# Optimization experiments

Measured on AMD Instinct MI355X. Metric: run time of the kernel, lower is better.

Reference implementation:

```python
import jax, jax.numpy as jnp
import numpy as np

E4M3_MAX = 448.0  # fp8_max_fwd for Format.HYBRID fprop tensors
MARGIN = 0        # DelayedScaling default


def _quantize_e4m3(t, s):
    # cast_to_fp8: scale, saturate-cast to E4M3; amax of the unscaled tensor
    q = (t * s).astype(jnp.float8_e4m3fn)
    amax = jnp.max(jnp.abs(t))
    return q, amax


def _sf_compute(amax, scale, fp8_max, margin):
    # faithful port of _default_sf_compute (including its tf.where ordering)
    exp = jnp.floor(jnp.log2(fp8_max / amax)) - margin
    sf = jnp.round(jnp.exp2(jnp.abs(exp)))
    sf = jnp.where(amax > 0.0, sf, scale)
    sf = jnp.where(jnp.isinf(amax), sf, scale)
    sf = jnp.where(exp < 0, 1.0 / sf, sf)
    return sf


def setup_inputs() -> dict:
    key = jax.random.key(0)
    k1, k2 = jax.random.split(key)
    M, K, N = 16384, 2048, 2048
    x = jax.random.normal(k1, (M, K), dtype=jnp.float32)
    kernel = jax.random.normal(k2, (K, N), dtype=jnp.float32) * 0.02
    scale = jnp.ones((2,), dtype=jnp.float32)
    scale_inv = jnp.ones((2,), dtype=jnp.float32)
    amax_history = jnp.zeros((1, 2), dtype=jnp.float32)
    return {"x": x, "kernel": kernel, "scale": scale,
            "scale_inv": scale_inv, "amax_history": amax_history}


def reference(x, kernel, scale, scale_inv, amax_history):
    # --- cast_to_fp8 for activation (index 0) and weight (index 1) ---
    x_q, amax_x = _quantize_e4m3(x, scale[0])          # [M, K] fp8
    w_q, amax_w = _quantize_e4m3(kernel.T, scale[1])   # [N, K] fp8 (B in row-major, gemm does B^T)
    new_scale_inv = jnp.stack([1.0 / scale[0], 1.0 / scale[1]])
    # record amaxes into most-recent slot of the history
    amax_history = amax_history.at[0, 0].set(amax_x).at[0, 1].set(amax_w)

    # --- fp8_matmul: D = (A * A_scale_inv) @ (B * B_scale_inv)^T ---
    out = jnp.matmul(x_q.astype(jnp.float32), w_q.astype(jnp.float32).T)
    out = out * (new_scale_inv[0] * new_scale_inv[1])  # [M, N]

    # --- fused_amax_and_scale_update (amax_compute_algo='most_recent') ---
    amax = amax_history[0]
    rolled = jnp.roll(amax_history, -1, axis=0).at[0].set(0.0)
    new_scale = _sf_compute(amax, scale, E4M3_MAX, MARGIN)
    return out, new_scale, rolled
```

## Files before the change

kernel.cpp:

```cpp
#include <hip/hip_runtime.h>
#include <cstdint>

#define M_DIM 16384
#define K_DIM 2048
#define N_DIM 2048

typedef float f32x4 __attribute__((ext_vector_type(4)));
typedef int   i32x8 __attribute__((ext_vector_type(8)));

__global__ __launch_bounds__(256) void quant_x_kernel(
    const float4* __restrict__ x, uint4* __restrict__ xq,
    const float* __restrict__ scale, unsigned int* __restrict__ amax)
{
    const int gid = blockIdx.x * 256 + threadIdx.x;
    const float s = scale[0];
    float m = 0.0f;
#pragma unroll
    for (int j = 0; j < 8; ++j) {
        float4 v = x[gid + j * 1048576];
        m = fmaxf(m, fmaxf(fmaxf(fabsf(v.x), fabsf(v.y)),
                           fmaxf(fabsf(v.z), fabsf(v.w))));
        unsigned int p0 = __builtin_amdgcn_cvt_pk_fp8_f32(v.x * s, v.y * s, 0, false);
        unsigned int p  = __builtin_amdgcn_cvt_pk_fp8_f32(v.z * s, v.w * s, p0, true);
        ((unsigned int*)xq)[gid + j * 1048576] = p;
    }

#pragma unroll
    for (int off = 32; off > 0; off >>= 1)
        m = fmaxf(m, __shfl_down(m, off, 64));
    __shared__ float red[4];
    if ((threadIdx.x & 63) == 0) red[threadIdx.x >> 6] = m;
    __syncthreads();
    if (threadIdx.x == 0) {
        m = fmaxf(fmaxf(red[0], red[1]), fmaxf(red[2], red[3]));
        atomicMax(amax, __float_as_uint(m));
    }
}

__global__ __launch_bounds__(256) void quant_w_kernel(
    const float* __restrict__ w, uint8_t* __restrict__ wq,
    const float* __restrict__ scale, unsigned int* __restrict__ amax)
{
    __shared__ float tile[64][68];
    const int t = threadIdx.x;
    const int nb = blockIdx.x * 64;
    const int kb = blockIdx.y * 64;
    const float s = scale[1];
    float m = 0.0f;
#pragma unroll
    for (int j = 0; j < 4; ++j) {
        int f = j * 256 + t;
        int row = f >> 4;
        int c4 = f & 15;
        float4 v = *(const float4*)(w + (size_t)(kb + row) * N_DIM + nb + c4 * 4);
        m = fmaxf(m, fmaxf(fmaxf(fabsf(v.x), fabsf(v.y)),
                           fmaxf(fabsf(v.z), fabsf(v.w))));
        *(float4*)(&tile[row][c4 * 4]) = v;
    }
    __syncthreads();
    const int n = t >> 2, c = t & 3;
    unsigned int pk[4];
#pragma unroll
    for (int jj = 0; jj < 4; ++jj) {
        float f0 = tile[c * 16 + jj * 4 + 0][n] * s;
        float f1 = tile[c * 16 + jj * 4 + 1][n] * s;
        float f2 = tile[c * 16 + jj * 4 + 2][n] * s;
        float f3 = tile[c * 16 + jj * 4 + 3][n] * s;
        unsigned int p = __builtin_amdgcn_cvt_pk_fp8_f32(f0, f1, 0, false);
        pk[jj] = __builtin_amdgcn_cvt_pk_fp8_f32(f2, f3, p, true);
    }
    *(uint4*)(wq + (size_t)(nb + n) * K_DIM + kb + c * 16) = make_uint4(pk[0], pk[1], pk[2], pk[3]);

#pragma unroll
    for (int off = 32; off > 0; off >>= 1)
        m = fmaxf(m, __shfl_down(m, off, 64));
    __shared__ float red[4];
    if ((t & 63) == 0) red[t >> 6] = m;
    __syncthreads();
    if (t == 0) {
        m = fmaxf(fmaxf(red[0], red[1]), fmaxf(red[2], red[3]));
        atomicMax(amax, __float_as_uint(m));
    }
}

__global__ __launch_bounds__(256) void gemm_fp8_kernel(
    const uint8_t* __restrict__ Aq, const uint8_t* __restrict__ Bq,
    const float* __restrict__ scale, float* __restrict__ C)
{
    __shared__ uint8_t lA[16384];
    __shared__ uint8_t lB[16384];
    const int tid  = threadIdx.x;
    const int wave = tid >> 6;
    const int lane = tid & 63;
    const int wm = wave >> 1, wn = wave & 1;
    const int q = lane >> 4, r = lane & 15;

    const int bn = blockIdx.x;
    const int bm = blockIdx.y;
    const size_t a_base = (size_t)bm * 128 * K_DIM;
    const size_t b_base = (size_t)bn * 128 * K_DIM;

    int srow[4], skoff[4], sdst[4];
#pragma unroll
    for (int j = 0; j < 4; ++j) {
        const int s  = j * 4 + wave;
        const int g  = s >> 1, hh = s & 1;
        const int fl = hh * 32 + (lane >> 1);
        srow[j]  = g * 16 + (fl & 15);
        skoff[j] = (fl >> 4) * 32 + (lane & 1) * 16;
        sdst[j]  = s * 1024 + lane * 16;
    }

    f32x4 acc[4][4];
#pragma unroll
    for (int i = 0; i < 4; ++i)
#pragma unroll
        for (int j = 0; j < 4; ++j) acc[i][j] = (f32x4){0.f, 0.f, 0.f, 0.f};

    const int SONE = 0x7F7F7F7F;

    for (int kt = 0; kt < K_DIM / 128; ++kt) {
        __syncthreads();
        const size_t kg = (size_t)kt * 128;
#pragma unroll
        for (int j = 0; j < 4; ++j) {
            const uint8_t* ga = Aq + a_base + (size_t)srow[j] * K_DIM + kg + skoff[j];
            const uint8_t* gb = Bq + b_base + (size_t)srow[j] * K_DIM + kg + skoff[j];
            __builtin_amdgcn_global_load_lds(
                (const __attribute__((address_space(1))) uint32_t*)ga,
                (__attribute__((address_space(3))) uint32_t*)(lA + sdst[j]), 16, 0, 0);
            __builtin_amdgcn_global_load_lds(
                (const __attribute__((address_space(1))) uint32_t*)gb,
                (__attribute__((address_space(3))) uint32_t*)(lB + sdst[j]), 16, 0, 0);
        }
        __syncthreads();

        i32x8 a_frag[4], b_frag[4];
#pragma unroll
        for (int mi = 0; mi < 4; ++mi) {
            const uint8_t* pa = lA + (wm * 4 + mi) * 2048 + lane * 32;
            int4 lo = *(const int4*)pa;
            int4 hi = *(const int4*)(pa + 16);
            a_frag[mi] = (i32x8){lo.x, lo.y, lo.z, lo.w, hi.x, hi.y, hi.z, hi.w};
        }
#pragma unroll
        for (int ni = 0; ni < 4; ++ni) {
            const uint8_t* pb = lB + (wn * 4 + ni) * 2048 + lane * 32;
            int4 lo = *(const int4*)pb;
            int4 hi = *(const int4*)(pb + 16);
            b_frag[ni] = (i32x8){lo.x, lo.y, lo.z, lo.w, hi.x, hi.y, hi.z, hi.w};
        }
#pragma unroll
        for (int mi = 0; mi < 4; ++mi)
#pragma unroll
            for (int ni = 0; ni < 4; ++ni)
                acc[mi][ni] = __builtin_amdgcn_mfma_scale_f32_16x16x128_f8f6f4(
                    a_frag[mi], b_frag[ni], acc[mi][ni],
                    0 , 0 ,
                    0, SONE, 0, SONE);
    }

    const float sinv = (1.0f / scale[0]) * (1.0f / scale[1]);
#pragma unroll
    for (int mi = 0; mi < 4; ++mi) {
#pragma unroll
        for (int ni = 0; ni < 4; ++ni) {
            const int col  = bn * 128 + wn * 64 + ni * 16 + r;
            const int row0 = bm * 128 + wm * 64 + mi * 16 + q * 4;
#pragma unroll
            for (int rr = 0; rr < 4; ++rr)
                C[(size_t)(row0 + rr) * N_DIM + col] = acc[mi][ni][rr] * sinv;
        }
    }
}

__global__ void finalize_kernel(const float* __restrict__ scale,
                                const unsigned int* __restrict__ amax_bits,
                                float* __restrict__ out_tail)
{
    const int i = threadIdx.x;
    if (i < 2) {
        const float amax = __uint_as_float(amax_bits[i]);
        const float sc = scale[i];
        const float e = floorf(log2f(448.0f / amax));
        float sf = roundf(exp2f(fabsf(e)));
        sf = (amax > 0.0f) ? sf : sc;
        sf = isinf(amax) ? sf : sc;
        if (e < 0.0f) sf = 1.0f / sf;
        out_tail[i] = sf;
        out_tail[2 + i] = 0.0f;
    }
}

extern "C" void kernel_launch(void* const* d_in, const int* in_sizes, int n_in,
                              void* d_out, int out_size, void* d_ws, size_t ws_size,
                              hipStream_t stream)
{
    const float* x     = (const float*)d_in[0];
    const float* w     = (const float*)d_in[1];
    const float* scale = (const float*)d_in[2];

    uint8_t* ws = (uint8_t*)d_ws;
    uint8_t* xq = ws;
    uint8_t* wq = ws + (size_t)M_DIM * K_DIM;
    unsigned int* amax = (unsigned int*)(ws + (size_t)M_DIM * K_DIM + (size_t)N_DIM * K_DIM);

    hipMemsetAsync(amax, 0, 2 * sizeof(unsigned int), stream);

    quant_x_kernel<<<4096, 256, 0, stream>>>(
        (const float4*)x, (uint4*)xq, scale, amax);

    dim3 gw(N_DIM / 64, K_DIM / 64);
    quant_w_kernel<<<gw, 256, 0, stream>>>(w, wq, scale, amax + 1);

    dim3 gg(N_DIM / 128, M_DIM / 128);
    gemm_fp8_kernel<<<gg, 256, 0, stream>>>(xq, wq, scale, (float*)d_out);

    finalize_kernel<<<1, 64, 0, stream>>>(scale, amax,
                                          (float*)d_out + (size_t)M_DIM * N_DIM);
}
```

Measured before the change: 349.3 us.

## Double-buffer LDS in FP8 GEMM, remap blocks per XCD, use nontemporal stores

The FP8 GEMM now uses two LDS stages. The next K-tile's global-to-LDS loads are issued before the MFMAs run on the current tile, so memory latency can overlap with compute. The staging layout is rearranged so each lane reads its fragment as two 16-byte chunks 1024 bytes apart, which is meant to reduce LDS bank conflicts. A 1D grid is remapped so that blocks on the same XCD share A row tiles for better L2 reuse, and output stores become nontemporal. The cost is doubling LDS to 64KB per block, which lowers occupancy, and the compiler may insert conservative vmcnt waits that limit the overlap.

```diff
diff --git a/kernel.cpp b/kernel.cpp
--- a/kernel.cpp
+++ b/kernel.cpp
@@ -87,27 +87,28 @@
     const uint8_t* __restrict__ Aq, const uint8_t* __restrict__ Bq,
     const float* __restrict__ scale, float* __restrict__ C)
 {
-    __shared__ uint8_t lA[16384];
-    __shared__ uint8_t lB[16384];
+    __shared__ uint8_t lds[65536];
     const int tid  = threadIdx.x;
     const int wave = tid >> 6;
     const int lane = tid & 63;
     const int wm = wave >> 1, wn = wave & 1;
     const int q = lane >> 4, r = lane & 15;
 
-    const int bn = blockIdx.x;
-    const int bm = blockIdx.y;
+    const int blk = blockIdx.x;
+    const int xcd = blk & 7;
+    const int idx = blk >> 3;
+    const int bm  = xcd * 16 + (idx >> 4);
+    const int bn  = idx & 15;
+
     const size_t a_base = (size_t)bm * 128 * K_DIM;
     const size_t b_base = (size_t)bn * 128 * K_DIM;
 
     int srow[4], skoff[4], sdst[4];
 #pragma unroll
     for (int j = 0; j < 4; ++j) {
-        const int s  = j * 4 + wave;
-        const int g  = s >> 1, hh = s & 1;
-        const int fl = hh * 32 + (lane >> 1);
-        srow[j]  = g * 16 + (fl & 15);
-        skoff[j] = (fl >> 4) * 32 + (lane & 1) * 16;
+        const int s = j * 4 + wave;
+        srow[j]  = (s >> 1) * 16 + (lane & 15);
+        skoff[j] = (lane >> 4) * 32 + (s & 1) * 16;
         sdst[j]  = s * 1024 + lane * 16;
     }
 
@@ -119,35 +120,42 @@
 
     const int SONE = 0x7F7F7F7F;
 
-    for (int kt = 0; kt < K_DIM / 128; ++kt) {
-        __syncthreads();
+    auto issue = [&](int kt, int b) {
         const size_t kg = (size_t)kt * 128;
+        uint8_t* base = lds + b * 32768;
 #pragma unroll
         for (int j = 0; j < 4; ++j) {
             const uint8_t* ga = Aq + a_base + (size_t)srow[j] * K_DIM + kg + skoff[j];
             const uint8_t* gb = Bq + b_base + (size_t)srow[j] * K_DIM + kg + skoff[j];
             __builtin_amdgcn_global_load_lds(
                 (const __attribute__((address_space(1))) uint32_t*)ga,
-                (__attribute__((address_space(3))) uint32_t*)(lA + sdst[j]), 16, 0, 0);
+                (__attribute__((address_space(3))) uint32_t*)(base + sdst[j]), 16, 0, 0);
             __builtin_amdgcn_global_load_lds(
                 (const __attribute__((address_space(1))) uint32_t*)gb,
-                (__attribute__((address_space(3))) uint32_t*)(lB + sdst[j]), 16, 0, 0);
-        }
+                (__attribute__((address_space(3))) uint32_t*)(base + 16384 + sdst[j]), 16, 0, 0);
+        }
+    };
+
+    issue(0, 0);
+
+    for (int kt = 0; kt < K_DIM / 128; ++kt) {
         __syncthreads();
-
+        if (kt + 1 < K_DIM / 128) issue(kt + 1, (kt + 1) & 1);
+
+        const uint8_t* base = lds + (kt & 1) * 32768;
         i32x8 a_frag[4], b_frag[4];
 #pragma unroll
         for (int mi = 0; mi < 4; ++mi) {
-            const uint8_t* pa = lA + (wm * 4 + mi) * 2048 + lane * 32;
+            const uint8_t* pa = base + (wm * 4 + mi) * 2048 + lane * 16;
             int4 lo = *(const int4*)pa;
-            int4 hi = *(const int4*)(pa + 16);
+            int4 hi = *(const int4*)(pa + 1024);
             a_frag[mi] = (i32x8){lo.x, lo.y, lo.z, lo.w, hi.x, hi.y, hi.z, hi.w};
         }
 #pragma unroll
         for (int ni = 0; ni < 4; ++ni) {
-            const uint8_t* pb = lB + (wn * 4 + ni) * 2048 + lane * 32;
+            const uint8_t* pb = base + 16384 + (wn * 4 + ni) * 2048 + lane * 16;
             int4 lo = *(const int4*)pb;
-            int4 hi = *(const int4*)(pb + 16);
+            int4 hi = *(const int4*)(pb + 1024);
             b_frag[ni] = (i32x8){lo.x, lo.y, lo.z, lo.w, hi.x, hi.y, hi.z, hi.w};
         }
 #pragma unroll
@@ -169,7 +177,8 @@
             const int row0 = bm * 128 + wm * 64 + mi * 16 + q * 4;
 #pragma unroll
             for (int rr = 0; rr < 4; ++rr)
-                C[(size_t)(row0 + rr) * N_DIM + col] = acc[mi][ni][rr] * sinv;
+                __builtin_nontemporal_store(acc[mi][ni][rr] * sinv,
+                    &C[(size_t)(row0 + rr) * N_DIM + col]);
         }
     }
 }
@@ -213,8 +222,7 @@
     dim3 gw(N_DIM / 64, K_DIM / 64);
     quant_w_kernel<<<gw, 256, 0, stream>>>(w, wq, scale, amax + 1);
 
-    dim3 gg(N_DIM / 128, M_DIM / 128);
-    gemm_fp8_kernel<<<gg, 256, 0, stream>>>(xq, wq, scale, (float*)d_out);
+    gemm_fp8_kernel<<<2048, 256, 0, stream>>>(xq, wq, scale, (float*)d_out);
 
     finalize_kernel<<<1, 64, 0, stream>>>(scale, amax,
                                           (float*)d_out + (size_t)M_DIM * N_DIM);
```

Measured after the change: 382.4 us. 9.5% more time.
